# Kernel tuning notes

Measured on AMD Instinct MI355X. Metric: run time of the kernel, lower is better.

The kernel has to match this reference:

```python
import jax, jax.numpy as jnp
import numpy as np

N_NODES = 20000
N_EDGES = 160000
N_GRAPHS = 64
VOCAB = 2 ** 16
EMBED_DIM = 32
IN_GNN = EMBED_DIM + 4  # 36
H1, H2 = 2048, 1024
N_CLASSES = 2  # task 'a'


def setup_inputs() -> dict:
    key = jax.random.key(0)
    ks = jax.random.split(key, 16)
    inp = {
        "node_type_ids": jax.random.randint(ks[0], (N_NODES,), 0, VOCAB, dtype=jnp.int32),
        "other_feats": jax.random.normal(ks[1], (N_NODES, 4), dtype=jnp.float32),
        "edge_index": jax.random.randint(ks[2], (2, N_EDGES), 0, N_NODES, dtype=jnp.int32),
        "batch": jnp.sort(jax.random.randint(ks[3], (N_NODES,), 0, N_GRAPHS, dtype=jnp.int32)),
        # parameters
        "emb": jax.random.normal(ks[4], (VOCAB, EMBED_DIM), dtype=jnp.float32),
        "W1": jax.random.normal(ks[5], (IN_GNN, H1), dtype=jnp.float32) * 0.05,
        "b1": jnp.zeros((H1,), jnp.float32),
        "W2": jax.random.normal(ks[6], (H1, H2), dtype=jnp.float32) * 0.02,
        "b2": jnp.zeros((H2,), jnp.float32),
        "hW1": jax.random.normal(ks[7], (H2, 1024), dtype=jnp.float32) * 0.02,
        "hb1": jnp.zeros((1024,), jnp.float32),
        "hW2": jax.random.normal(ks[8], (1024, 512), dtype=jnp.float32) * 0.02,
        "hb2": jnp.zeros((512,), jnp.float32),
        "oW": jax.random.normal(ks[9], (512, N_CLASSES), dtype=jnp.float32) * 0.02,
        "ob": jnp.zeros((N_CLASSES,), jnp.float32),
    }
    return inp


def _gcn_conv(x, W, b, src, dst, dinv):
    # PyG GCNConv (add_self_loops already applied in src/dst, dinv precomputed):
    # out_i = sum_{j->i} dinv[j]*dinv[i] * (x_j @ W) + b
    xw = x @ W  # [N, out]
    norm = dinv[src] * dinv[dst]  # [E']
    msg = xw[src] * norm[:, None]  # [E', out] -- dominant HBM traffic
    out = jax.ops.segment_sum(msg, dst, num_segments=x.shape[0])
    return out + b


def _forward(node_type_ids, other_feats, edge_index, batch,
             emb, W1, b1, W2, b2, hW1, hb1, hW2, hb2, oW, ob):
    n = other_feats.shape[0]
    # add self-loops (gcn_norm default)
    loop = jnp.arange(n, dtype=edge_index.dtype)
    src = jnp.concatenate([edge_index[0], loop])
    dst = jnp.concatenate([edge_index[1], loop])
    deg = jax.ops.segment_sum(jnp.ones(src.shape[0], other_feats.dtype), dst, num_segments=n)
    dinv = jnp.where(deg > 0, jax.lax.rsqrt(deg), 0.0)

    x = jnp.concatenate([emb[node_type_ids], other_feats], axis=-1)  # [N, 36]
    x = jax.nn.relu(_gcn_conv(x, W1, b1, src, dst, dinv))  # dropout is eval no-op
    x = jax.nn.relu(_gcn_conv(x, W2, b2, src, dst, dinv))

    # global mean pool over graphs
    counts = jax.ops.segment_sum(jnp.ones(n, x.dtype), batch, num_segments=N_GRAPHS)
    pooled = jax.ops.segment_sum(x, batch, num_segments=N_GRAPHS)
    pooled = pooled / jnp.maximum(counts, 1.0)[:, None]  # [G, 1024]

    h = jax.nn.relu(pooled @ hW1 + hb1)
    h = jax.nn.relu(h @ hW2 + hb2)
    return h @ oW + ob  # [G, 2]


def reference(node_type_ids, other_feats, edge_index, batch,
              emb, W1, b1, W2, b2, hW1, hb1, hW2, hb2, oW, ob):
    return _forward(node_type_ids, other_feats, edge_index, batch,
                    emb, W1, b1, W2, b2, hW1, hb1, hW2, hb2, oW, ob)
```

## Files before the change

### kernel.cpp

```cpp
#include <hip/hip_runtime.h>
#include <hip/hip_bf16.h>

#define N_NODES  20000
#define N_EDGES  160000
#define N_TOT_E  180000
#define N_GRAPHS 64
#define EMBED_DIM 32
#define IN_GNN   36
#define K1PAD    64
#define H1       2048
#define H2       1024
#define NPANELS  157

typedef unsigned short u16;
typedef short bf16x8 __attribute__((ext_vector_type(8)));
typedef float f32x4  __attribute__((ext_vector_type(4)));
typedef _Float16 f16;
typedef f16  f16x8  __attribute__((ext_vector_type(8)));

__device__ inline u16 f32_to_bf16(float f) {
    union { float f; unsigned u; } v; v.f = f;
    unsigned lsb = (v.u >> 16) & 1u;
    return (u16)((v.u + 0x7fffu + lsb) >> 16);
}
__device__ inline float bf16_to_f32(u16 h) {
    union { unsigned u; float f; } v; v.u = ((unsigned)h) << 16;
    return v.f;
}
__device__ inline u16 f16_bits(f16 h) { union { f16 h; u16 u; } v; v.h = h; return v.u; }


__global__ void fill_i32(int* p, int v, int n) {
    int i = blockIdx.x * 256 + threadIdx.x;
    if (i < n) p[i] = v;
}

__global__ void deg_accum(const int* __restrict__ ei, int* indeg) {
    int e = blockIdx.x * 256 + threadIdx.x;
    if (e < N_EDGES) atomicAdd(&indeg[ei[N_EDGES + e]], 1);
}

__global__ void deg_to_dinv(const int* __restrict__ indeg, float* __restrict__ d) {
    int i = blockIdx.x * 256 + threadIdx.x;
    if (i < N_NODES) d[i] = rsqrtf((float)indeg[i]);
}

__global__ void build_xfeat(const int* __restrict__ ids, const float* __restrict__ other,
                            const float* __restrict__ emb, float* __restrict__ xf) {
    int idx = blockIdx.x * 256 + threadIdx.x;
    if (idx >= N_NODES * IN_GNN) return;
    int i = idx / IN_GNN;
    int d = idx - i * IN_GNN;
    float v = (d < EMBED_DIM) ? emb[(size_t)ids[i] * EMBED_DIM + d]
                              : other[i * 4 + (d - EMBED_DIM)];
    xf[idx] = v;
}

__global__ __launch_bounds__(1024) void scan_offsets(const int* __restrict__ indeg,
                                                     int* __restrict__ off,
                                                     int* __restrict__ cursor) {
    __shared__ int buf[1024];
    __shared__ int base_s;
    int tid = threadIdx.x;
    if (tid == 0) base_s = 0;
    __syncthreads();
    for (int start = 0; start < N_NODES; start += 1024) {
        int i = start + tid;
        int v = (i < N_NODES) ? indeg[i] : 0;
        buf[tid] = v;
        __syncthreads();
        for (int s = 1; s < 1024; s <<= 1) {
            int t = (tid >= s) ? buf[tid - s] : 0;
            __syncthreads();
            buf[tid] += t;
            __syncthreads();
        }
        int incl = buf[tid];
        int excl = incl - v;
        int base = base_s;
        if (i < N_NODES) {
            int o = base + excl;
            off[i] = o;
            cursor[i] = o;
        }
        __syncthreads();
        if (tid == 1023) base_s = base + incl;
        __syncthreads();
    }
    if (tid == 0) off[N_NODES] = N_TOT_E;
}

__global__ void csr_fill(const int* __restrict__ ei, const float* __restrict__ dinv,
                         int* __restrict__ cursor,
                         int* __restrict__ csr_src, float* __restrict__ csr_nrm) {
    int e = blockIdx.x * 256 + threadIdx.x;
    if (e >= N_TOT_E) return;
    int s, t;
    if (e < N_EDGES) { s = ei[e]; t = ei[N_EDGES + e]; }
    else             { s = t = e - N_EDGES; }
    int pos = atomicAdd(&cursor[t], 1);
    csr_src[pos] = s;
    csr_nrm[pos] = dinv[s] * dinv[t];
}

__global__ void agg_csr_36(const int* __restrict__ off, const int* __restrict__ csr_src,
                           const float* __restrict__ csr_nrm,
                           const float* __restrict__ xf,
                           u16* __restrict__ aggh, u16* __restrict__ aggl) {
    int idx = blockIdx.x * 256 + threadIdx.x;
    if (idx >= N_NODES * K1PAD) return;
    int node = idx >> 6;
    int d = idx & 63;
    u16 hi = 0, lo = 0;
    if (d < IN_GNN) {
        int p0 = off[node], p1 = off[node + 1];
        float acc = 0.0f;
        for (int p = p0; p < p1; p++)
            acc += xf[csr_src[p] * IN_GNN + d] * csr_nrm[p];
        hi = f32_to_bf16(acc);
        lo = f32_to_bf16(acc - bf16_to_f32(hi));
    }
    aggh[idx] = hi;
    aggl[idx] = lo;
}

__global__ void conv_w1(const float* __restrict__ W,
                        u16* __restrict__ Bh, u16* __restrict__ Bl) {
    int idx = blockIdx.x * 256 + threadIdx.x;
    if (idx >= H1 * K1PAD) return;
    int n = idx >> 6;
    int k = idx & 63;
    u16 hi = 0, lo = 0;
    if (k < IN_GNN) {
        float v = W[(size_t)k * H1 + n];
        hi = f32_to_bf16(v);
        lo = f32_to_bf16(v - bf16_to_f32(hi));
    }
    Bh[idx] = hi;
    Bl[idx] = lo;
}

__global__ __launch_bounds__(256) void conv_w2(const float* __restrict__ W,
                                               u16* __restrict__ Bh,
                                               u16* __restrict__ Bl) {
    __shared__ float t[32][33];
    int bk = blockIdx.x * 32;
    int bn = blockIdx.y * 32;
    int tx = threadIdx.x & 31, ty = threadIdx.x >> 5;
#pragma unroll
    for (int i = 0; i < 32; i += 8)
        t[ty + i][tx] = W[(size_t)(bk + ty + i) * H2 + bn + tx];
    __syncthreads();
#pragma unroll
    for (int i = 0; i < 32; i += 8) {
        float v = t[tx][ty + i];
        f16 h = (f16)v;
        f16 l = (f16)(v - (float)h);
        size_t o = (size_t)(bn + ty + i) * H1 + bk + tx;
        Bh[o] = f16_bits(h);
        Bl[o] = f16_bits(l);
    }
}

__global__ __launch_bounds__(256) void gemm1_mfma(const u16* __restrict__ Ah,
                                                  const u16* __restrict__ Al,
                                                  const u16* __restrict__ Bh,
                                                  const u16* __restrict__ Bl,
                                                  const float* __restrict__ bias,
                                                  u16* __restrict__ Xf) {
    __shared__ __align__(16) u16 lds[4][128 * K1PAD];
    const int tid  = threadIdx.x;
    const int wid  = tid >> 6;
    const int lane = tid & 63;
    const int wr   = wid >> 1, wc = wid & 1;
    const int row0 = blockIdx.y * 128;
    const int col0 = blockIdx.x * 128;

    const u16* gbase;
    int rbase; bool isA;
    if      (wid == 0) { gbase = Ah; rbase = row0; isA = true; }
    else if (wid == 1) { gbase = Al; rbase = row0; isA = true; }
    else if (wid == 2) { gbase = Bh; rbase = col0; isA = false; }
    else               { gbase = Bl; rbase = col0; isA = false; }
    u16* myl = lds[wid];
    const int r_l  = lane >> 3;
    const int ks_l = (lane & 7) * 8;
#pragma unroll
    for (int i = 0; i < 16; i++) {
        int r = rbase + i * 8 + r_l;
        if (isA && r > N_NODES - 1) r = N_NODES - 1;
        const u16* g = gbase + (size_t)r * K1PAD + ks_l;
        __builtin_amdgcn_global_load_lds(
            (const __attribute__((address_space(1))) void*)g,
            (__attribute__((address_space(3))) void*)(myl + i * 512),
            16, 0, 0);
    }
    __syncthreads();

    f32x4 acc[4][4] = {};
#pragma unroll
    for (int ks = 0; ks < 2; ks++) {
        bf16x8 afh[4], afl[4];
#pragma unroll
        for (int mi = 0; mi < 4; mi++) {
            int r   = wr * 64 + mi * 16 + (lane & 15);
            int off = r * K1PAD + ks * 32 + (lane >> 4) * 8;
            afh[mi] = *(const bf16x8*)&lds[0][off];
            afl[mi] = *(const bf16x8*)&lds[1][off];
        }
#pragma unroll
        for (int ni = 0; ni < 4; ni++) {
            int c   = wc * 64 + ni * 16 + (lane & 15);
            int off = c * K1PAD + ks * 32 + (lane >> 4) * 8;
            bf16x8 bfh = *(const bf16x8*)&lds[2][off];
            bf16x8 bfl = *(const bf16x8*)&lds[3][off];
#pragma unroll
            for (int mi = 0; mi < 4; mi++) {
                acc[mi][ni] = __builtin_amdgcn_mfma_f32_16x16x32_bf16(afh[mi], bfh, acc[mi][ni], 0, 0, 0);
                acc[mi][ni] = __builtin_amdgcn_mfma_f32_16x16x32_bf16(afh[mi], bfl, acc[mi][ni], 0, 0, 0);
                acc[mi][ni] = __builtin_amdgcn_mfma_f32_16x16x32_bf16(afl[mi], bfh, acc[mi][ni], 0, 0, 0);
            }
        }
    }

    __syncthreads();
    float (*ldsF)[128] = (float (*)[128])(&lds[0][0]);
#pragma unroll
    for (int ni = 0; ni < 4; ni++) {
        int colL = wc * 64 + ni * 16 + (lane & 15);
        float bb = bias[col0 + colL];
#pragma unroll
        for (int mi = 0; mi < 4; mi++) {
#pragma unroll
            for (int j = 0; j < 4; j++) {
                int rowL = wr * 64 + mi * 16 + (lane >> 4) * 4 + j;
                ldsF[rowL][colL] = fmaxf(acc[mi][ni][j] + bb, 0.0f);
            }
        }
    }
    __syncthreads();
    int rL = tid >> 1;
    int cb = (tid & 1) * 8;
    int lr = row0 + rL;
    if (lr < N_NODES) {
        size_t gb = (size_t)lr * H1 + col0;
#pragma unroll
        for (int c = 0; c < 8; c++) {
            int col = c * 16 + cb;
            u16 hv[8];
#pragma unroll
            for (int e = 0; e < 8; e++)
                hv[e] = f16_bits((f16)ldsF[rL][col + e]);
            *(f16x8*)&Xf[gb + col] = *(f16x8*)hv;
        }
    }
}

__global__ __launch_bounds__(256) void gemm2_mfma(const u16* __restrict__ Af,
                                                  const u16* __restrict__ Bh,
                                                  const u16* __restrict__ Bl,
                                                  float* __restrict__ C) {
    __shared__ u16 ldsA[128 * 32], ldsBh[128 * 32], ldsBl[128 * 32];
    const int tid  = threadIdx.x;
    const int wid  = tid >> 6;
    const int lane = tid & 63;
    const int wr   = wid >> 1, wc = wid & 1;

    int NB = (int)(gridDim.x * gridDim.y);
    int b  = (int)(blockIdx.y * gridDim.x + blockIdx.x);
    int lin = (b & 7) * (NB >> 3) + (b >> 3);
    const int col0 = (lin & 7) * 128;
    const int row0 = (lin >> 3) * 128;

    const u16* gbase;
    u16* mybase;
    int rbase, niter;
    if      (wid == 0) { gbase = Af; mybase = ldsA;          rbase = row0;      niter = 4; }
    else if (wid == 1) { gbase = Af; mybase = ldsA + 2048;   rbase = row0 + 64; niter = 4; }
    else if (wid == 2) { gbase = Bh; mybase = ldsBh;         rbase = col0;      niter = 8; }
    else               { gbase = Bl; mybase = ldsBl;         rbase = col0;      niter = 8; }
    const int r_l  = lane >> 2;
    const int ks_l = (lane & 3) * 8;

    int rows[8];
#pragma unroll
    for (int i = 0; i < 8; i++) {
        int r = rbase + i * 16 + r_l;
        if (wid < 2 && r > N_NODES - 1) r = N_NODES - 1;
        rows[i] = r;
    }

    f32x4 acc[4][4] = {};

    for (int kt = 0; kt < H1 / 32; ++kt) {
        int k0 = kt * 32;
        __syncthreads();
        for (int i = 0; i < niter; i++) {
            const u16* g = gbase + (size_t)rows[i] * H1 + k0 + ks_l;
            __builtin_amdgcn_global_load_lds(
                (const __attribute__((address_space(1))) void*)g,
                (__attribute__((address_space(3))) void*)(mybase + i * 512),
                16, 0, 0);
        }
        __syncthreads();

        f16x8 af[4];
#pragma unroll
        for (int mi = 0; mi < 4; mi++) {
            int r   = wr * 64 + mi * 16 + (lane & 15);
            int off = r * 32 + (lane >> 4) * 8;
            af[mi] = *(const f16x8*)&ldsA[off];
        }
#pragma unroll
        for (int ni = 0; ni < 4; ni++) {
            int c   = wc * 64 + ni * 16 + (lane & 15);
            int off = c * 32 + (lane >> 4) * 8;
            f16x8 bfh = *(const f16x8*)&ldsBh[off];
            f16x8 bfl = *(const f16x8*)&ldsBl[off];
#pragma unroll
            for (int mi = 0; mi < 4; mi++) {
                acc[mi][ni] = __builtin_amdgcn_mfma_f32_16x16x32_f16(af[mi], bfh, acc[mi][ni], 0, 0, 0);
                acc[mi][ni] = __builtin_amdgcn_mfma_f32_16x16x32_f16(af[mi], bfl, acc[mi][ni], 0, 0, 0);
            }
        }
    }

#pragma unroll
    for (int mi = 0; mi < 4; mi++) {
#pragma unroll
        for (int ni = 0; ni < 4; ni++) {
            int col = col0 + wc * 64 + ni * 16 + (lane & 15);
#pragma unroll
            for (int j = 0; j < 4; j++) {
                int lr = row0 + wr * 64 + mi * 16 + (lane >> 4) * 4 + j;
                if (lr < N_NODES) C[(size_t)lr * H2 + col] = acc[mi][ni][j];
            }
        }
    }
}

__global__ __launch_bounds__(256) void agg_csr_1024(const int* __restrict__ off,
                                                    const int* __restrict__ csr_src,
                                                    const float* __restrict__ csr_nrm,
                                                    const float* __restrict__ xw,
                                                    const float* __restrict__ b,
                                                    float* __restrict__ x2) {
    int node = blockIdx.x;
    int p0 = off[node], p1 = off[node + 1];
    int d = threadIdx.x;
    float4 a0 = make_float4(0.f, 0.f, 0.f, 0.f);
    float4 a1 = make_float4(0.f, 0.f, 0.f, 0.f);
    int p = p0;
    for (; p + 1 < p1; p += 2) {
        int   s0 = csr_src[p],     s1 = csr_src[p + 1];
        float n0 = csr_nrm[p],     n1 = csr_nrm[p + 1];
        float4 v0 = ((const float4*)&xw[(size_t)s0 * H2])[d];
        float4 v1 = ((const float4*)&xw[(size_t)s1 * H2])[d];
        a0.x += v0.x * n0; a0.y += v0.y * n0; a0.z += v0.z * n0; a0.w += v0.w * n0;
        a1.x += v1.x * n1; a1.y += v1.y * n1; a1.z += v1.z * n1; a1.w += v1.w * n1;
    }
    if (p < p1) {
        int   s0 = csr_src[p];
        float n0 = csr_nrm[p];
        float4 v0 = ((const float4*)&xw[(size_t)s0 * H2])[d];
        a0.x += v0.x * n0; a0.y += v0.y * n0; a0.z += v0.z * n0; a0.w += v0.w * n0;
    }
    float4 bb = ((const float4*)b)[d];
    float4 o;
    o.x = fmaxf(a0.x + a1.x + bb.x, 0.f);
    o.y = fmaxf(a0.y + a1.y + bb.y, 0.f);
    o.z = fmaxf(a0.z + a1.z + bb.z, 0.f);
    o.w = fmaxf(a0.w + a1.w + bb.w, 0.f);
    ((float4*)&x2[(size_t)node * H2])[d] = o;
}

__global__ void cnt_accum(const int* __restrict__ batch, float* cnt) {
    int i = blockIdx.x * 256 + threadIdx.x;
    if (i < N_NODES) atomicAdd(&cnt[batch[i]], 1.0f);
}

__global__ void pool_accum(const int* __restrict__ batch, const float* __restrict__ x2,
                           float* __restrict__ pooled) {
    int d  = blockIdx.x * 256 + threadIdx.x;
    int i0 = blockIdx.y * 64;
    float acc = 0.0f;
    int gprev = -1;
    for (int i = 0; i < 64; i++) {
        int node = i0 + i;
        if (node >= N_NODES) break;
        int g = batch[node];
        if (g != gprev) {
            if (gprev >= 0) atomicAdd(&pooled[gprev * H2 + d], acc);
            acc = 0.0f; gprev = g;
        }
        acc += x2[(size_t)node * H2 + d];
    }
    if (gprev >= 0) atomicAdd(&pooled[gprev * H2 + d], acc);
}

__global__ void pool_norm(float* pooled, const float* cnt) {
    int idx = blockIdx.x * 256 + threadIdx.x;
    if (idx < N_GRAPHS * H2) {
        int g = idx >> 10;
        pooled[idx] /= fmaxf(cnt[g], 1.0f);
    }
}

__global__ __launch_bounds__(256) void head_gemm(const float* __restrict__ In,
                                                 const float* __restrict__ W,
                                                 float* __restrict__ Out, int K, int N) {
    __shared__ __align__(16) float As[16][256];
    int n  = blockIdx.x * 256 + threadIdx.x;
    int m0 = blockIdx.y * 16;
    int k0 = blockIdx.z * 256;
    for (int t = threadIdx.x; t < 16 * 256; t += 256) {
        int r = t >> 8, k = t & 255;
        As[r][k] = In[(size_t)(m0 + r) * K + k0 + k];
    }
    __syncthreads();
    float acc[16] = {};
    for (int k = 0; k < 256; k += 4) {
        float w0 = W[(size_t)(k0 + k + 0) * N + n];
        float w1 = W[(size_t)(k0 + k + 1) * N + n];
        float w2 = W[(size_t)(k0 + k + 2) * N + n];
        float w3 = W[(size_t)(k0 + k + 3) * N + n];
#pragma unroll
        for (int r = 0; r < 16; r++) {
            float4 a = *(const float4*)&As[r][k];
            acc[r] += a.x * w0 + a.y * w1 + a.z * w2 + a.w * w3;
        }
    }
    for (int r = 0; r < 16; r++)
        atomicAdd(&Out[(size_t)(m0 + r) * N + n], acc[r]);
}

__global__ void bias_relu_MN(float* __restrict__ x, const float* __restrict__ b,
                             int N, int total) {
    int idx = blockIdx.x * 256 + threadIdx.x;
    if (idx < total) {
        int d = idx & (N - 1);
        x[idx] = fmaxf(x[idx] + b[d], 0.0f);
    }
}

__global__ void head3(const float* __restrict__ h2, const float* __restrict__ oW,
                      const float* __restrict__ ob, float* __restrict__ out) {
    int tid = threadIdx.x;
    if (tid >= 128) return;
    int m = tid >> 1, c = tid & 1;
    float acc = 0.0f;
    for (int k = 0; k < 512; k++) acc += h2[m * 512 + k] * oW[k * 2 + c];
    out[tid] = acc + ob[c];
}

extern "C" void kernel_launch(void* const* d_in, const int* in_sizes, int n_in,
                              void* d_out, int out_size, void* d_ws, size_t ws_size,
                              hipStream_t stream) {
    const int*   ids   = (const int*)d_in[0];
    const float* other = (const float*)d_in[1];
    const int*   ei    = (const int*)d_in[2];
    const int*   batch = (const int*)d_in[3];
    const float* emb   = (const float*)d_in[4];
    const float* W1    = (const float*)d_in[5];
    const float* b1    = (const float*)d_in[6];
    const float* W2    = (const float*)d_in[7];
    const float* b2    = (const float*)d_in[8];
    const float* hW1   = (const float*)d_in[9];
    const float* hb1   = (const float*)d_in[10];
    const float* hW2   = (const float*)d_in[11];
    const float* hb2   = (const float*)d_in[12];
    const float* oW    = (const float*)d_in[13];
    const float* ob    = (const float*)d_in[14];
    float* out = (float*)d_out;

    char* ws = (char*)d_ws;
    size_t off_b = 0;
    auto alloc = [&](size_t bytes) {
        size_t p = (off_b + 255) & ~(size_t)255;
        off_b = p + bytes;
        return p;
    };
    size_t o_dinv = alloc((size_t)N_NODES * 4);
    size_t o_indeg= alloc((size_t)(N_NODES + 1) * 4);
    size_t o_off  = alloc((size_t)(N_NODES + 1) * 4);
    size_t o_cur  = alloc((size_t)N_NODES * 4);
    size_t o_csrc = alloc((size_t)N_TOT_E * 4);
    size_t o_cnrm = alloc((size_t)N_TOT_E * 4);
    size_t o_xf   = alloc((size_t)N_NODES * IN_GNN * 4);
    size_t o_aggh = alloc((size_t)N_NODES * K1PAD * 2);
    size_t o_aggl = alloc((size_t)N_NODES * K1PAD * 2);
    size_t o_w1h  = alloc((size_t)H1 * K1PAD * 2);
    size_t o_w1l  = alloc((size_t)H1 * K1PAD * 2);
    size_t o_x1f  = alloc((size_t)N_NODES * H1 * 2);
    size_t o_w2h  = alloc((size_t)H2 * H1 * 2);
    size_t o_w2l  = alloc((size_t)H2 * H1 * 2);
    size_t o_xw2  = alloc((size_t)N_NODES * H2 * 4);
    size_t o_pool = alloc((size_t)N_GRAPHS * H2 * 4);
    size_t o_cnt  = alloc((size_t)N_GRAPHS * 4);
    size_t o_h1   = alloc((size_t)N_GRAPHS * 1024 * 4);
    size_t o_h2   = alloc((size_t)N_GRAPHS * 512 * 4);

    float* dinv = (float*)(ws + o_dinv);
    int*   indeg= (int*)(ws + o_indeg);
    int*   offs = (int*)(ws + o_off);
    int*   cur  = (int*)(ws + o_cur);
    int*   csrc = (int*)(ws + o_csrc);
    float* cnrm = (float*)(ws + o_cnrm);
    float* xf   = (float*)(ws + o_xf);
    u16*   aggh = (u16*)(ws + o_aggh);
    u16*   aggl = (u16*)(ws + o_aggl);
    u16*   w1h  = (u16*)(ws + o_w1h);
    u16*   w1l  = (u16*)(ws + o_w1l);
    u16*   x1f  = (u16*)(ws + o_x1f);
    u16*   w2h  = (u16*)(ws + o_w2h);
    u16*   w2l  = (u16*)(ws + o_w2l);
    float* xw2  = (float*)(ws + o_xw2);
    float* x2   = (float*)(ws + o_x1f);
    float* pooled = (float*)(ws + o_pool);
    float* cnt  = (float*)(ws + o_cnt);
    float* h1   = (float*)(ws + o_h1);
    float* h2   = (float*)(ws + o_h2);

    fill_i32<<<(N_NODES + 255) / 256, 256, 0, stream>>>(indeg, 1, N_NODES);
    deg_accum<<<(N_EDGES + 255) / 256, 256, 0, stream>>>(ei, indeg);
    deg_to_dinv<<<(N_NODES + 255) / 256, 256, 0, stream>>>(indeg, dinv);

    scan_offsets<<<1, 1024, 0, stream>>>(indeg, offs, cur);
    csr_fill<<<(N_TOT_E + 255) / 256, 256, 0, stream>>>(ei, dinv, cur, csrc, cnrm);

    build_xfeat<<<(N_NODES * IN_GNN + 255) / 256, 256, 0, stream>>>(ids, other, emb, xf);
    agg_csr_36<<<(N_NODES * K1PAD + 255) / 256, 256, 0, stream>>>(offs, csrc, cnrm, xf, aggh, aggl);

    conv_w1<<<(H1 * K1PAD + 255) / 256, 256, 0, stream>>>(W1, w1h, w1l);
    conv_w2<<<dim3(H1 / 32, H2 / 32), 256, 0, stream>>>(W2, w2h, w2l);

    gemm1_mfma<<<dim3(H1 / 128, NPANELS), 256, 0, stream>>>(aggh, aggl, w1h, w1l, b1, x1f);

    gemm2_mfma<<<dim3(H2 / 128, NPANELS), 256, 0, stream>>>(x1f, w2h, w2l, xw2);

    agg_csr_1024<<<N_NODES, 256, 0, stream>>>(offs, csrc, cnrm, xw2, b2, x2);

    hipMemsetAsync(pooled, 0, (size_t)N_GRAPHS * H2 * 4, stream);
    hipMemsetAsync(cnt, 0, (size_t)N_GRAPHS * 4, stream);
    cnt_accum<<<(N_NODES + 255) / 256, 256, 0, stream>>>(batch, cnt);
    pool_accum<<<dim3(H2 / 256, (N_NODES + 63) / 64), 256, 0, stream>>>(batch, x2, pooled);
    pool_norm<<<(N_GRAPHS * H2 + 255) / 256, 256, 0, stream>>>(pooled, cnt);

    hipMemsetAsync(h1, 0, (size_t)N_GRAPHS * 1024 * 4, stream);
    head_gemm<<<dim3(1024 / 256, 4, 1024 / 256), 256, 0, stream>>>(pooled, hW1, h1, 1024, 1024);
    bias_relu_MN<<<(N_GRAPHS * 1024 + 255) / 256, 256, 0, stream>>>(h1, hb1, 1024, N_GRAPHS * 1024);

    hipMemsetAsync(h2, 0, (size_t)N_GRAPHS * 512 * 4, stream);
    head_gemm<<<dim3(512 / 256, 4, 1024 / 256), 256, 0, stream>>>(h1, hW2, h2, 1024, 512);
    bias_relu_MN<<<(N_GRAPHS * 512 + 255) / 256, 256, 0, stream>>>(h2, hb2, 512, N_GRAPHS * 512);

    head3<<<1, 128, 0, stream>>>(h2, oW, ob, out);
}
```

Before: 839.3 us.

## Store layer-2 XW as fp16 and double GEMM2 K-tile to 64

GEMM2 now writes its output XW as fp16 rather than fp32, and the edge aggregation kernel reads fp16 and converts to float before accumulating. This halves the bytes written by the GEMM and the bytes gathered per edge in the 1024-wide aggregation, which is the dominant gather traffic. In addition, the GEMM K-tile grows from 32 to 64 with six LDS tiles and balanced load distribution across all four waves, halving the number of barriers. The cost is fp16 rounding and range limits on the intermediate XW values.

```diff
diff --git a/kernel.cpp b/kernel.cpp
--- a/kernel.cpp
+++ b/kernel.cpp
@@ -28,6 +28,7 @@
     return v.f;
 }
 __device__ inline u16 f16_bits(f16 h) { union { f16 h; u16 u; } v; v.h = h; return v.u; }
+__device__ inline float f16u_to_f32(u16 u) { union { u16 u; f16 h; } v; v.u = u; return (float)v.h; }
 
 
 __global__ void fill_i32(int* p, int v, int n) {
@@ -259,8 +260,8 @@
 __global__ __launch_bounds__(256) void gemm2_mfma(const u16* __restrict__ Af,
                                                   const u16* __restrict__ Bh,
                                                   const u16* __restrict__ Bl,
-                                                  float* __restrict__ C) {
-    __shared__ u16 ldsA[128 * 32], ldsBh[128 * 32], ldsBl[128 * 32];
+                                                  u16* __restrict__ C) {
+    __shared__ u16 lds[6][128 * 32];
     const int tid  = threadIdx.x;
     const int wid  = tid >> 6;
     const int lane = tid & 63;
@@ -272,55 +273,50 @@
     const int col0 = (lin & 7) * 128;
     const int row0 = (lin >> 3) * 128;
 
-    const u16* gbase;
-    u16* mybase;
-    int rbase, niter;
-    if      (wid == 0) { gbase = Af; mybase = ldsA;          rbase = row0;      niter = 4; }
-    else if (wid == 1) { gbase = Af; mybase = ldsA + 2048;   rbase = row0 + 64; niter = 4; }
-    else if (wid == 2) { gbase = Bh; mybase = ldsBh;         rbase = col0;      niter = 8; }
-    else               { gbase = Bl; mybase = ldsBl;         rbase = col0;      niter = 8; }
     const int r_l  = lane >> 2;
     const int ks_l = (lane & 3) * 8;
 
-    int rows[8];
-#pragma unroll
-    for (int i = 0; i < 8; i++) {
-        int r = rbase + i * 16 + r_l;
-        if (wid < 2 && r > N_NODES - 1) r = N_NODES - 1;
-        rows[i] = r;
-    }
-
     f32x4 acc[4][4] = {};
 
-    for (int kt = 0; kt < H1 / 32; ++kt) {
-        int k0 = kt * 32;
+    for (int kt = 0; kt < H1 / 64; ++kt) {
+        int k0 = kt * 64;
         __syncthreads();
-        for (int i = 0; i < niter; i++) {
-            const u16* g = gbase + (size_t)rows[i] * H1 + k0 + ks_l;
+        for (int u = wid * 12; u < wid * 12 + 12; u++) {
+            int tile = u >> 3;
+            int it   = u & 7;
+            int s    = tile & 1;
+            int t    = tile >> 1;
+            const u16* g = (t == 0) ? Af : (t == 1) ? Bh : Bl;
+            int r = ((t == 0) ? row0 : col0) + it * 16 + r_l;
+            if (t == 0 && r > N_NODES - 1) r = N_NODES - 1;
+            const u16* src = g + (size_t)r * H1 + k0 + s * 32 + ks_l;
             __builtin_amdgcn_global_load_lds(
-                (const __attribute__((address_space(1))) void*)g,
-                (__attribute__((address_space(3))) void*)(mybase + i * 512),
+                (const __attribute__((address_space(1))) void*)src,
+                (__attribute__((address_space(3))) void*)(&lds[tile][it * 512]),
                 16, 0, 0);
         }
         __syncthreads();
 
-        f16x8 af[4];
-#pragma unroll
-        for (int mi = 0; mi < 4; mi++) {
-            int r   = wr * 64 + mi * 16 + (lane & 15);
-            int off = r * 32 + (lane >> 4) * 8;
-            af[mi] = *(const f16x8*)&ldsA[off];
-        }
-#pragma unroll
-        for (int ni = 0; ni < 4; ni++) {
-            int c   = wc * 64 + ni * 16 + (lane & 15);
-            int off = c * 32 + (lane >> 4) * 8;
-            f16x8 bfh = *(const f16x8*)&ldsBh[off];
-            f16x8 bfl = *(const f16x8*)&ldsBl[off];
+#pragma unroll
+        for (int ks = 0; ks < 2; ks++) {
+            f16x8 af[4];
 #pragma unroll
             for (int mi = 0; mi < 4; mi++) {
-                acc[mi][ni] = __builtin_amdgcn_mfma_f32_16x16x32_f16(af[mi], bfh, acc[mi][ni], 0, 0, 0);
-                acc[mi][ni] = __builtin_amdgcn_mfma_f32_16x16x32_f16(af[mi], bfl, acc[mi][ni], 0, 0, 0);
+                int r   = wr * 64 + mi * 16 + (lane & 15);
+                int off = r * 32 + (lane >> 4) * 8;
+                af[mi] = *(const f16x8*)&lds[ks][off];
+            }
+#pragma unroll
+            for (int ni = 0; ni < 4; ni++) {
+                int c   = wc * 64 + ni * 16 + (lane & 15);
+                int off = c * 32 + (lane >> 4) * 8;
+                f16x8 bfh = *(const f16x8*)&lds[2 + ks][off];
+                f16x8 bfl = *(const f16x8*)&lds[4 + ks][off];
+#pragma unroll
+                for (int mi = 0; mi < 4; mi++) {
+                    acc[mi][ni] = __builtin_amdgcn_mfma_f32_16x16x32_f16(af[mi], bfh, acc[mi][ni], 0, 0, 0);
+                    acc[mi][ni] = __builtin_amdgcn_mfma_f32_16x16x32_f16(af[mi], bfl, acc[mi][ni], 0, 0, 0);
+                }
             }
         }
     }
@@ -333,7 +329,7 @@
 #pragma unroll
             for (int j = 0; j < 4; j++) {
                 int lr = row0 + wr * 64 + mi * 16 + (lane >> 4) * 4 + j;
-                if (lr < N_NODES) C[(size_t)lr * H2 + col] = acc[mi][ni][j];
+                if (lr < N_NODES) C[(size_t)lr * H2 + col] = f16_bits((f16)acc[mi][ni][j]);
             }
         }
     }
@@ -342,7 +338,7 @@
 __global__ __launch_bounds__(256) void agg_csr_1024(const int* __restrict__ off,
                                                     const int* __restrict__ csr_src,
                                                     const float* __restrict__ csr_nrm,
-                                                    const float* __restrict__ xw,
+                                                    const u16* __restrict__ xw,
                                                     const float* __restrict__ b,
                                                     float* __restrict__ x2) {
     int node = blockIdx.x;
@@ -354,16 +350,19 @@
     for (; p + 1 < p1; p += 2) {
         int   s0 = csr_src[p],     s1 = csr_src[p + 1];
         float n0 = csr_nrm[p],     n1 = csr_nrm[p + 1];
-        float4 v0 = ((const float4*)&xw[(size_t)s0 * H2])[d];
-        float4 v1 = ((const float4*)&xw[(size_t)s1 * H2])[d];
-        a0.x += v0.x * n0; a0.y += v0.y * n0; a0.z += v0.z * n0; a0.w += v0.w * n0;
-        a1.x += v1.x * n1; a1.y += v1.y * n1; a1.z += v1.z * n1; a1.w += v1.w * n1;
+        ushort4 v0 = ((const ushort4*)&xw[(size_t)s0 * H2])[d];
+        ushort4 v1 = ((const ushort4*)&xw[(size_t)s1 * H2])[d];
+        a0.x += f16u_to_f32(v0.x) * n0; a0.y += f16u_to_f32(v0.y) * n0;
+        a0.z += f16u_to_f32(v0.z) * n0; a0.w += f16u_to_f32(v0.w) * n0;
+        a1.x += f16u_to_f32(v1.x) * n1; a1.y += f16u_to_f32(v1.y) * n1;
+        a1.z += f16u_to_f32(v1.z) * n1; a1.w += f16u_to_f32(v1.w) * n1;
     }
     if (p < p1) {
         int   s0 = csr_src[p];
         float n0 = csr_nrm[p];
-        float4 v0 = ((const float4*)&xw[(size_t)s0 * H2])[d];
-        a0.x += v0.x * n0; a0.y += v0.y * n0; a0.z += v0.z * n0; a0.w += v0.w * n0;
+        ushort4 v0 = ((const ushort4*)&xw[(size_t)s0 * H2])[d];
+        a0.x += f16u_to_f32(v0.x) * n0; a0.y += f16u_to_f32(v0.y) * n0;
+        a0.z += f16u_to_f32(v0.z) * n0; a0.w += f16u_to_f32(v0.w) * n0;
     }
     float4 bb = ((const float4*)b)[d];
     float4 o;
@@ -494,7 +493,7 @@
     size_t o_x1f  = alloc((size_t)N_NODES * H1 * 2);
     size_t o_w2h  = alloc((size_t)H2 * H1 * 2);
     size_t o_w2l  = alloc((size_t)H2 * H1 * 2);
-    size_t o_xw2  = alloc((size_t)N_NODES * H2 * 4);
+    size_t o_xw2  = alloc((size_t)N_NODES * H2 * 2);
     size_t o_pool = alloc((size_t)N_GRAPHS * H2 * 4);
     size_t o_cnt  = alloc((size_t)N_GRAPHS * 4);
     size_t o_h1   = alloc((size_t)N_GRAPHS * 1024 * 4);
@@ -514,7 +513,7 @@
     u16*   x1f  = (u16*)(ws + o_x1f);
     u16*   w2h  = (u16*)(ws + o_w2h);
     u16*   w2l  = (u16*)(ws + o_w2l);
-    float* xw2  = (float*)(ws + o_xw2);
+    u16*   xw2  = (u16*)(ws + o_xw2);
     float* x2   = (float*)(ws + o_x1f);
     float* pooled = (float*)(ws + o_pool);
     float* cnt  = (float*)(ws + o_cnt);
```

New measurement: 751.3 us. 10.5% less time.
